# Performance work log

Hardware: AMD Instinct MI355X
Metric: run time of the kernel (lower is better)

Reference implementation:

```python
import jax, jax.numpy as jnp
import numpy as np

N, E, CIN, COUT = 50000, 800000, 61, 64
EPS = 1e-5


def batchnorm(h, g, b):
    # BatchNorm1d in training mode: batch stats (biased variance), affine
    m = jnp.mean(h, axis=0)
    v = jnp.var(h, axis=0)
    return g * (h - m) * jax.lax.rsqrt(v + EPS) + b


def setup_inputs() -> dict:
    key = jax.random.key(0)
    ks = jax.random.split(key, 7)
    x = jax.random.normal(ks[0], (N, CIN), jnp.float32)
    pos = jax.random.normal(ks[1], (N, 3), jnp.float32)
    edge_index = jax.random.randint(ks[2], (2, E), 0, N, dtype=jnp.int64)
    s1 = 1.0 / np.sqrt(CIN + 3)
    s2 = 1.0 / np.sqrt(COUT)
    ss = 1.0 / np.sqrt(CIN)
    W1 = jax.random.normal(ks[3], (CIN + 3, COUT), jnp.float32) * s1
    b1 = jnp.zeros((COUT,), jnp.float32)
    W2 = jax.random.normal(ks[4], (COUT, COUT), jnp.float32) * s2
    b2 = jnp.zeros((COUT,), jnp.float32)
    Ws = jax.random.normal(ks[5], (CIN, COUT), jnp.float32) * ss
    bs = jnp.zeros((COUT,), jnp.float32)
    ones = jnp.ones((COUT,), jnp.float32)
    zeros = jnp.zeros((COUT,), jnp.float32)
    return {
        "x": x, "pos": pos, "edge_index": edge_index,
        "W1": W1, "b1": b1, "g1": ones, "be1": zeros,
        "W2": W2, "b2": b2, "g2": ones, "be2": zeros,
        "Ws": Ws, "bs": bs, "gs": ones, "bes": zeros,
        "gf": ones, "bef": zeros,
    }


def reference(x, pos, edge_index, W1, b1, g1, be1, W2, b2, g2, be2,
              Ws, bs, gs, bes, gf, bef):
    src, dst = edge_index[0], edge_index[1]  # j -> i (source_to_target)
    # per-edge message: [x_j, pos_j - pos_i]  -> [E, CIN+3]
    msg = jnp.concatenate([x[src], pos[src] - pos[dst]], axis=-1)
    # local_nn = MLP([CIN+3, COUT, COUT]) with per-layer Lin -> ReLU -> BN
    h = batchnorm(jax.nn.relu(msg @ W1 + b1), g1, be1)
    h = batchnorm(jax.nn.relu(h @ W2 + b2), g2, be2)
    # scatter-max aggregation to destination nodes
    agg = jax.ops.segment_max(h, dst, num_segments=N)
    agg = jnp.where(jnp.isneginf(agg), 0.0, agg)  # nodes with no incoming edges
    # residual shortcut (Linear + BN since CIN != COUT)
    identity = batchnorm(x @ Ws + bs, gs, bes)
    return jax.nn.relu(batchnorm(agg, gf, bef) + identity)
```

## Files before the change

kernel.cpp:

```cpp
#include <hip/hip_runtime.h>

#define CIN 61
constexpr float EPS = 1e-5f;
constexpr double SCALE = 16777216.0;

using s16x8 = __attribute__((ext_vector_type(8))) short;
using fx4   = __attribute__((ext_vector_type(4))) float;

static __device__ __forceinline__ unsigned short f2bf(float f) {
  unsigned int u = __float_as_uint(f);
  u = (u + 0x7fffu + ((u >> 16) & 1u)) >> 16;
  return (unsigned short)u;
}
static __device__ __forceinline__ float bf2f(unsigned short h) {
  return __uint_as_float(((unsigned int)h) << 16);
}

__device__ __forceinline__ void stat_reduce(float val, float* red, long long* dst_ll) {
  int tid = threadIdx.x;
  red[tid] = val;
  __syncthreads();
  if (tid < 64) {
    float t = red[tid] + red[tid + 64] + red[tid + 128] + red[tid + 192];
    atomicAdd((unsigned long long*)&dst_ll[tid],
              (unsigned long long)(long long)((double)t * SCALE));
  }
  __syncthreads();
}

__global__ __launch_bounds__(256) void k_node(
    const float* __restrict__ x, const float* __restrict__ W1,
    const float* __restrict__ b1, const float* __restrict__ Ws,
    const float* __restrict__ bs, unsigned short* __restrict__ y,
    unsigned short* __restrict__ s_out, long long* __restrict__ stats, int N,
    const int* __restrict__ ei, unsigned int* __restrict__ hist,
    unsigned short* __restrict__ rank, int E) {
  const int tid = threadIdx.x, lane = tid & 63, wv = tid >> 6;
  float w1r[64], wsr[64];
#pragma unroll
  for (int k = 0; k < 64; ++k) {
    w1r[k] = (k < CIN) ? W1[k * 64 + lane] : 0.f;
    wsr[k] = (k < CIN) ? Ws[k * 64 + lane] : 0.f;
  }
  const float b1v = b1[lane], bsv = bs[lane];
  __shared__ float lrow[4][64];
  __shared__ float red[256];
  float ssum = 0.f, ssq = 0.f;
  const int nq = N >> 2;
  for (int q = blockIdx.x; q < nq; q += gridDim.x) {
    const int n = (q << 2) + wv;
    lrow[wv][lane] = (lane < CIN) ? x[(size_t)n * CIN + lane] : 0.f;
    __builtin_amdgcn_wave_barrier();
    float a0 = b1v, a1 = 0.f, a2 = 0.f, a3 = 0.f;
    float c0 = bsv, c1 = 0.f, c2 = 0.f, c3 = 0.f;
    const float4* rr = (const float4*)&lrow[wv][0];
#pragma unroll
    for (int k4 = 0; k4 < 16; ++k4) {
      float4 v = rr[k4];
      a0 = fmaf(v.x, w1r[4 * k4 + 0], a0);
      a1 = fmaf(v.y, w1r[4 * k4 + 1], a1);
      a2 = fmaf(v.z, w1r[4 * k4 + 2], a2);
      a3 = fmaf(v.w, w1r[4 * k4 + 3], a3);
      c0 = fmaf(v.x, wsr[4 * k4 + 0], c0);
      c1 = fmaf(v.y, wsr[4 * k4 + 1], c1);
      c2 = fmaf(v.z, wsr[4 * k4 + 2], c2);
      c3 = fmaf(v.w, wsr[4 * k4 + 3], c3);
    }
    y[(size_t)n * 64 + lane] = f2bf((a0 + a1) + (a2 + a3));
    const float sacc = (c0 + c1) + (c2 + c3);
    s_out[(size_t)n * 64 + lane] = f2bf(sacc);
    ssum += sacc;
    ssq = fmaf(sacc, sacc, ssq);
    __builtin_amdgcn_wave_barrier();
  }
  stat_reduce(ssum, red, stats + 256);
  stat_reduce(ssq, red, stats + 320);
  for (int i = blockIdx.x * 256 + tid; i < E; i += gridDim.x * 256) {
    const int dst = ei[E + i];
    rank[i] = (unsigned short)atomicAdd(&hist[dst], 1u);
  }
}

__global__ __launch_bounds__(256) void k_scan1(
    const unsigned int* __restrict__ hist, unsigned int* __restrict__ bsum) {
  const int tid = threadIdx.x, lane = tid & 63, wv = tid >> 6;
  const uint4 v = ((const uint4*)(hist + blockIdx.x * 1024))[tid];
  unsigned int s = v.x + v.y + v.z + v.w;
#pragma unroll
  for (int off = 1; off < 64; off <<= 1) s += __shfl_xor(s, off);
  __shared__ unsigned int wsum[4];
  if (lane == 0) wsum[wv] = s;
  __syncthreads();
  if (tid == 0) bsum[blockIdx.x] = wsum[0] + wsum[1] + wsum[2] + wsum[3];
}

__global__ void k_scan2(const unsigned int* __restrict__ bsum,
                        unsigned int* __restrict__ boff, int nb) {
  const int t = threadIdx.x;
  unsigned int v = (t < nb) ? bsum[t] : 0u;
  unsigned int incl = v;
#pragma unroll
  for (int off = 1; off < 64; off <<= 1) {
    unsigned int u = __shfl_up(incl, off);
    if (t >= off) incl += u;
  }
  if (t < nb) boff[t] = incl - v;
}

__global__ __launch_bounds__(256) void k_scan3(
    const unsigned int* __restrict__ hist, const unsigned int* __restrict__ boff,
    unsigned int* __restrict__ cursor0) {
  const int tid = threadIdx.x, lane = tid & 63, wv = tid >> 6;
  const uint4 v = ((const uint4*)(hist + blockIdx.x * 1024))[tid];
  const unsigned int s = v.x + v.y + v.z + v.w;
  unsigned int incl = s;
#pragma unroll
  for (int off = 1; off < 64; off <<= 1) {
    unsigned int u = __shfl_up(incl, off);
    if (lane >= off) incl += u;
  }
  __shared__ unsigned int wtot[4];
  if (lane == 63) wtot[wv] = incl;
  __syncthreads();
  unsigned int wb = boff[blockIdx.x];
#pragma unroll
  for (int k = 0; k < 4; ++k) wb += (k < wv) ? wtot[k] : 0u;
  const unsigned int ex = wb + incl - s;
  uint4 o;
  o.x = ex; o.y = ex + v.x; o.z = o.y + v.y; o.w = o.z + v.z;
  ((uint4*)(cursor0 + blockIdx.x * 1024))[tid] = o;
}

__global__ __launch_bounds__(256) void k_dstfill(
    const unsigned int* __restrict__ cursor0, unsigned short* __restrict__ dstS,
    int N) {
  const int d = blockIdx.x * 256 + threadIdx.x;
  if (d >= N) return;
  const unsigned int lo = cursor0[d];
  const unsigned int hi = cursor0[d + 1];
  for (unsigned int i = lo; i < hi; ++i) dstS[i] = (unsigned short)d;
}

__global__ __launch_bounds__(256) void k_edge1(
    const int* __restrict__ ei, const float* __restrict__ pos,
    const unsigned short* __restrict__ y, const float* __restrict__ W1,
    const unsigned int* __restrict__ cursor0, const unsigned short* __restrict__ rank,
    unsigned short* __restrict__ t1S, long long* __restrict__ stats, int E) {
  const int tid = threadIdx.x, lane = tid & 63, wv = tid >> 6;
  const int g8 = lane >> 3, c8 = lane & 7;
  float wp[3][8];
#pragma unroll
  for (int d = 0; d < 3; ++d)
#pragma unroll
    for (int i = 0; i < 8; ++i) wp[d][i] = W1[(61 + d) * 64 + 8 * c8 + i];
  float ssum[8] = {0.f, 0.f, 0.f, 0.f, 0.f, 0.f, 0.f, 0.f};
  float ssq[8]  = {0.f, 0.f, 0.f, 0.f, 0.f, 0.f, 0.f, 0.f};
  const int ngrp = E >> 3;
  const int nw = gridDim.x * 4;
  for (int q = blockIdx.x * 4 + wv; q < ngrp; q += 4 * nw) {
    const int qB = q + nw, qC = q + 2 * nw, qD = q + 3 * nw;
    const bool hB = qB < ngrp, hC = qC < ngrp, hD = qD < ngrp;
    const int eA = (q << 3) + g8;
    const int eB = hB ? (qB << 3) + g8 : eA;
    const int eC = hC ? (qC << 3) + g8 : eA;
    const int eD = hD ? (qD << 3) + g8 : eA;
    const int srcA = ei[eA], dstA = ei[E + eA];
    const int srcB = ei[eB], dstB = ei[E + eB];
    const int srcC = ei[eC], dstC = ei[E + eC];
    const int srcD = ei[eD], dstD = ei[E + eD];
    float pvA = 0.f, pvB = 0.f, pvC = 0.f, pvD = 0.f;
    if (c8 < 3) {
      pvA = pos[srcA * 3 + c8] - pos[dstA * 3 + c8];
      pvB = pos[srcB * 3 + c8] - pos[dstB * 3 + c8];
      pvC = pos[srcC * 3 + c8] - pos[dstC * 3 + c8];
      pvD = pos[srcD * 3 + c8] - pos[dstD * 3 + c8];
    }
    const s16x8 yA = *(const s16x8*)(y + (unsigned)srcA * 64u + 8u * (unsigned)c8);
    const s16x8 yB = *(const s16x8*)(y + (unsigned)srcB * 64u + 8u * (unsigned)c8);
    const s16x8 yC = *(const s16x8*)(y + (unsigned)srcC * 64u + 8u * (unsigned)c8);
    const s16x8 yD = *(const s16x8*)(y + (unsigned)srcD * 64u + 8u * (unsigned)c8);
    unsigned offA = 0, offB = 0, offC = 0, offD = 0;
    if (c8 == 0) {
      offA = cursor0[dstA] + rank[eA];
      offB = cursor0[dstB] + rank[eB];
      offC = cursor0[dstC] + rank[eC];
      offD = cursor0[dstD] + rank[eD];
    }
#define EDGE1_BODY(PV, YV, OFFV)                                                \
    {                                                                           \
      const float p0 = __shfl(PV, g8 * 8 + 0);                                  \
      const float p1 = __shfl(PV, g8 * 8 + 1);                                  \
      const float p2 = __shfl(PV, g8 * 8 + 2);                                  \
      const unsigned off = __shfl(OFFV, g8 * 8 + 0);                            \
      union { s16x8 v; unsigned short s[8]; } tb;                               \
      _Pragma("unroll")                                                         \
      for (int i = 0; i < 8; ++i) {                                             \
        float v = bf2f((unsigned short)YV[i]);                                  \
        v = fmaf(p0, wp[0][i], v);                                              \
        v = fmaf(p1, wp[1][i], v);                                              \
        v = fmaf(p2, wp[2][i], v);                                              \
        v = fmaxf(v, 0.f);                                                      \
        ssum[i] += v;                                                           \
        ssq[i] = fmaf(v, v, ssq[i]);                                            \
        tb.s[i] = f2bf(v);                                                      \
      }                                                                         \
      *(s16x8*)(t1S + (size_t)off * 64 + 8 * c8) = tb.v;                        \
    }
    EDGE1_BODY(pvA, yA, offA)
    if (hB) EDGE1_BODY(pvB, yB, offB)
    if (hC) EDGE1_BODY(pvC, yC, offC)
    if (hD) EDGE1_BODY(pvD, yD, offD)
#undef EDGE1_BODY
  }
#pragma unroll
  for (int i = 0; i < 8; ++i) {
    ssum[i] += __shfl_xor(ssum[i], 8);
    ssum[i] += __shfl_xor(ssum[i], 16);
    ssum[i] += __shfl_xor(ssum[i], 32);
    ssq[i] += __shfl_xor(ssq[i], 8);
    ssq[i] += __shfl_xor(ssq[i], 16);
    ssq[i] += __shfl_xor(ssq[i], 32);
  }
  __shared__ float sred[2][64];
  if (tid < 128) ((float*)sred)[tid] = 0.f;
  __syncthreads();
  if (g8 == 0) {
#pragma unroll
    for (int i = 0; i < 8; ++i) {
      atomicAdd(&sred[0][8 * c8 + i], ssum[i]);
      atomicAdd(&sred[1][8 * c8 + i], ssq[i]);
    }
  }
  __syncthreads();
  if (tid < 64) {
    atomicAdd((unsigned long long*)&stats[0 + tid],
              (unsigned long long)(long long)((double)sred[0][tid] * SCALE));
    atomicAdd((unsigned long long*)&stats[64 + tid],
              (unsigned long long)(long long)((double)sred[1][tid] * SCALE));
  }
}

__global__ void k_coefA(const long long* __restrict__ stats,
                        const float* __restrict__ g1, const float* __restrict__ be1,
                        const float* __restrict__ W2, const float* __restrict__ b2,
                        unsigned short* __restrict__ bFpack,
                        float* __restrict__ biasF, double invE) {
  const int c = threadIdx.x;
  __shared__ float a1s[64], c1s[64], b2sh[64];
  double m = (double)stats[c] * invE;
  double v = (double)stats[64 + c] * invE - m * m;
  float a = g1[c] * rsqrtf((float)v + EPS);
  a1s[c] = a;
  c1s[c] = fmaf(-(float)m, a, be1[c]);
  __syncthreads();
  float acc = b2[c];
  for (int k = 0; k < 64; ++k) acc = fmaf(c1s[k], W2[k * 64 + c], acc);
  b2sh[c] = acc;
  const int lg = c >> 4, l15 = c & 15;
#pragma unroll
  for (int t = 0; t < 4; ++t)
#pragma unroll
    for (int s = 0; s < 2; ++s)
#pragma unroll
      for (int i = 0; i < 8; ++i) {
        const int k = s * 32 + lg * 8 + i;
        bFpack[c * 64 + t * 16 + s * 8 + i] = f2bf(a1s[k] * W2[k * 64 + l15 + 16 * t]);
      }
  __syncthreads();
  float4 bf;
  bf.x = b2sh[l15]; bf.y = b2sh[l15 + 16]; bf.z = b2sh[l15 + 32]; bf.w = b2sh[l15 + 48];
  ((float4*)biasF)[c] = bf;
}

__global__ __launch_bounds__(256) void k_edge2(
    const unsigned short* __restrict__ t1S, const unsigned short* __restrict__ dstS,
    const unsigned short* __restrict__ bFpack, const float* __restrict__ biasF,
    long long* __restrict__ stats, unsigned int* __restrict__ agg, int E) {
  const int tid = threadIdx.x, lane = tid & 63, wv = tid >> 6;
  const int l15 = lane & 15, lg = lane >> 4;
  s16x8 bF[4][2];
  {
    const s16x8* bfp = (const s16x8*)(bFpack + (size_t)lane * 64);
#pragma unroll
    for (int t = 0; t < 4; ++t)
#pragma unroll
      for (int s = 0; s < 2; ++s) bF[t][s] = bfp[t * 2 + s];
  }
  float bias[4];
  {
    const float4 bv = ((const float4*)biasF)[lane];
    bias[0] = bv.x; bias[1] = bv.y; bias[2] = bv.z; bias[3] = bv.w;
  }
  __shared__ float ld2[4][16][68];
  float ssum[4] = {0.f, 0.f, 0.f, 0.f}, ssq[4] = {0.f, 0.f, 0.f, 0.f};
  const int nchunk = E >> 6;
  const int nw4 = gridDim.x * 4;
  for (int ch = blockIdx.x * 4 + wv; ch < nchunk; ch += nw4) {
    const int row0 = ch << 6;
    int cur = -1;
    float m = 0.f;
    bool inside = false;
#pragma unroll
    for (int t4 = 0; t4 < 4; ++t4) {
      const int rbase = row0 + (t4 << 4);
      const unsigned short* ar = t1S + (size_t)(rbase + l15) * 64 + (unsigned)(lg * 8);
      const s16x8 aF0 = *(const s16x8*)ar;
      const s16x8 aF1 = *(const s16x8*)(ar + 32);
      const int dstv = (int)dstS[rbase + l15];
      fx4 acc[4];
#pragma unroll
      for (int t = 0; t < 4; ++t) {
        acc[t][0] = bias[t]; acc[t][1] = bias[t];
        acc[t][2] = bias[t]; acc[t][3] = bias[t];
      }
#pragma unroll
      for (int t = 0; t < 4; ++t) {
        acc[t] = __builtin_amdgcn_mfma_f32_16x16x32_bf16(aF0, bF[t][0], acc[t], 0, 0, 0);
        acc[t] = __builtin_amdgcn_mfma_f32_16x16x32_bf16(aF1, bF[t][1], acc[t], 0, 0, 0);
      }
#pragma unroll
      for (int t = 0; t < 4; ++t) {
        const int col = l15 + 16 * t;
#pragma unroll
        for (int j = 0; j < 4; ++j) {
          const float v = fmaxf(acc[t][j], 0.f);
          ssum[t] += v;
          ssq[t] = fmaf(v, v, ssq[t]);
          ld2[wv][lg * 4 + j][col] = v;
        }
      }
      __builtin_amdgcn_wave_barrier();
      float v16[16];
#pragma unroll
      for (int r = 0; r < 16; ++r) v16[r] = ld2[wv][r][lane];
#pragma unroll
      for (int r = 0; r < 16; ++r) {
        const int d = __shfl(dstv, r);
        const float v = v16[r];
        if (d == cur) {
          m = fmaxf(m, v);
        } else {
          if (cur >= 0) {
            const unsigned int enc = __float_as_uint(m) | 0x80000000u;
            if (inside) agg[(unsigned)cur * 64u + lane] = enc;
            else atomicMax(&agg[(unsigned)cur * 64u + lane], enc);
          }
          cur = d;
          m = v;
          inside = (t4 > 0) || (r > 0);
        }
      }
      __builtin_amdgcn_wave_barrier();
    }
    if (cur >= 0)
      atomicMax(&agg[(unsigned)cur * 64u + lane], __float_as_uint(m) | 0x80000000u);
  }
#pragma unroll
  for (int t = 0; t < 4; ++t) {
    ssum[t] += __shfl_xor(ssum[t], 16); ssum[t] += __shfl_xor(ssum[t], 32);
    ssq[t]  += __shfl_xor(ssq[t], 16);  ssq[t]  += __shfl_xor(ssq[t], 32);
  }
  __shared__ float sred[2][64];
  if (tid < 128) ((float*)sred)[tid] = 0.f;
  __syncthreads();
  if (lg == 0) {
#pragma unroll
    for (int t = 0; t < 4; ++t) {
      atomicAdd(&sred[0][l15 + 16 * t], ssum[t]);
      atomicAdd(&sred[1][l15 + 16 * t], ssq[t]);
    }
  }
  __syncthreads();
  if (tid < 64) {
    atomicAdd((unsigned long long*)&stats[128 + tid],
              (unsigned long long)(long long)((double)sred[0][tid] * SCALE));
    atomicAdd((unsigned long long*)&stats[192 + tid],
              (unsigned long long)(long long)((double)sred[1][tid] * SCALE));
  }
}

__global__ __launch_bounds__(256) void k_aggfix(
    const unsigned int* __restrict__ agg, long long* __restrict__ stats, int total) {
  const int tid = threadIdx.x;
  __shared__ float red[256];
  float ssum = 0.f, ssq = 0.f, kcf = 0.f;
  const int step = gridDim.x * 256;
  for (int i = blockIdx.x * 256 + tid; i < total; i += step) {
    const unsigned int u = agg[i];
    if (u >> 31) {
      const float v = __uint_as_float(u & 0x7fffffffu);
      ssum += v;
      ssq = fmaf(v, v, ssq);
      if ((i & 63) == 0) kcf += 1.f;
    }
  }
  stat_reduce(ssum, red, stats + 384);
  stat_reduce(ssq, red, stats + 448);
  stat_reduce(kcf, red, stats + 512);
}

__global__ void k_coefB(const long long* __restrict__ stats,
                        const float* __restrict__ g2, const float* __restrict__ be2,
                        const float* __restrict__ gs, const float* __restrict__ bes,
                        const float* __restrict__ gf, const float* __restrict__ bef,
                        float* __restrict__ coef, double invE, double invN, int N) {
  const int c = threadIdx.x;
  double m2 = (double)stats[128 + c] * invE;
  double v2 = (double)stats[192 + c] * invE - m2 * m2;
  float a2 = g2[c] * rsqrtf((float)v2 + EPS);
  float c2 = fmaf(-(float)m2, a2, be2[c]);
  double mS = (double)stats[256 + c] * invN;
  double vS = (double)stats[320 + c] * invN - mS * mS;
  float aS = gs[c] * rsqrtf((float)vS + EPS);
  float cS = fmaf(-(float)mS, aS, bes[c]);
  double su = (double)stats[384 + c] / SCALE;
  double qu = (double)stats[448 + c] / SCALE;
  double K  = (double)stats[512] / SCALE;
  double sv = (double)a2 * su + (double)c2 * K;
  double qv = (double)a2 * a2 * qu + 2.0 * a2 * c2 * su + (double)c2 * c2 * K;
  double mv = sv / N;
  double vv = qv / N - mv * mv;
  float aF = gf[c] * rsqrtf((float)vv + EPS);
  float cF = fmaf(-(float)mv, aF, bef[c]);
  coef[c]       = aF * a2;
  coef[64 + c]  = fmaf(aF, c2, cF);
  coef[128 + c] = cF;
  coef[192 + c] = aS;
  coef[256 + c] = cS;
}

__global__ __launch_bounds__(256) void k_final(
    const unsigned int* __restrict__ agg, const unsigned short* __restrict__ sbuf,
    const float* __restrict__ coef, float* __restrict__ out, int total) {
  int i = blockIdx.x * 256 + threadIdx.x;
  if (i >= total) return;
  const int c = i & 63;
  const unsigned int u = agg[i];
  float base;
  if (u >> 31)
    base = fmaf(coef[c], __uint_as_float(u & 0x7fffffffu), coef[64 + c]);
  else
    base = coef[128 + c];
  const float sv = fmaf(coef[192 + c], bf2f(sbuf[i]), coef[256 + c]);
  out[i] = fmaxf(base + sv, 0.f);
}

extern "C" void kernel_launch(void* const* d_in, const int* in_sizes, int n_in,
                              void* d_out, int out_size, void* d_ws, size_t ws_size,
                              hipStream_t stream) {
  const float* x   = (const float*)d_in[0];
  const float* pos = (const float*)d_in[1];
  const int*   ei  = (const int*)d_in[2];
  const float* W1  = (const float*)d_in[3];
  const float* b1  = (const float*)d_in[4];
  const float* g1  = (const float*)d_in[5];
  const float* be1 = (const float*)d_in[6];
  const float* W2  = (const float*)d_in[7];
  const float* b2  = (const float*)d_in[8];
  const float* g2  = (const float*)d_in[9];
  const float* be2 = (const float*)d_in[10];
  const float* Ws  = (const float*)d_in[11];
  const float* bs  = (const float*)d_in[12];
  const float* gs  = (const float*)d_in[13];
  const float* bes = (const float*)d_in[14];
  const float* gf  = (const float*)d_in[15];
  const float* bef = (const float*)d_in[16];
  const int N = in_sizes[0] / CIN;
  const int E = in_sizes[2] / 2;

  char* ws = (char*)d_ws;
  const size_t o_stats = 0;
  const size_t o_bsum  = 4608;
  const size_t o_boff  = 5120;
  const size_t o_hist  = 8192;
  const size_t o_agg   = o_hist + 200704;
  const size_t zeroEnd = o_agg + (size_t)N * 256;
  const size_t o_curs0 = zeroEnd;
  const size_t o_coef  = o_curs0 + 200704;
  const size_t o_frag  = o_coef + 4096;
  const size_t o_rank  = o_frag + 12288;
  const size_t o_dstS  = o_rank + (size_t)E * 2;
  const size_t o_ybuf  = o_dstS + (size_t)E * 2;
  const size_t o_sbuf  = o_ybuf + (size_t)N * 128;
  const size_t o_t1S   = o_sbuf + (size_t)N * 128;

  long long* stats      = (long long*)(ws + o_stats);
  unsigned int* bsum    = (unsigned int*)(ws + o_bsum);
  unsigned int* boff    = (unsigned int*)(ws + o_boff);
  unsigned int* hist    = (unsigned int*)(ws + o_hist);
  unsigned int* agg     = (unsigned int*)(ws + o_agg);
  unsigned int* cursor0 = (unsigned int*)(ws + o_curs0);
  float* coef           = (float*)(ws + o_coef);
  unsigned short* bFpack= (unsigned short*)(ws + o_frag);
  float* biasF          = (float*)(ws + o_frag + 8192);
  unsigned short* rank  = (unsigned short*)(ws + o_rank);
  unsigned short* dstS  = (unsigned short*)(ws + o_dstS);
  unsigned short* ybuf  = (unsigned short*)(ws + o_ybuf);
  unsigned short* sbuf  = (unsigned short*)(ws + o_sbuf);
  unsigned short* t1S   = (unsigned short*)(ws + o_t1S);

  const double invE = 1.0 / (SCALE * (double)E);
  const double invN = 1.0 / (SCALE * (double)N);
  const int total = N * 64;
  const int nScanBlk = 49;

  hipMemsetAsync(d_ws, 0, zeroEnd, stream);

  hipLaunchKernelGGL(k_node, dim3(1024), dim3(256), 0, stream,
                     x, W1, b1, Ws, bs, ybuf, sbuf, stats, N, ei, hist, rank, E);
  hipLaunchKernelGGL(k_scan1, dim3(nScanBlk), dim3(256), 0, stream, hist, bsum);
  hipLaunchKernelGGL(k_scan2, dim3(1), dim3(64), 0, stream, bsum, boff, nScanBlk);
  hipLaunchKernelGGL(k_scan3, dim3(nScanBlk), dim3(256), 0, stream,
                     hist, boff, cursor0);
  hipLaunchKernelGGL(k_dstfill, dim3((N + 255) / 256), dim3(256), 0, stream,
                     cursor0, dstS, N);
  hipLaunchKernelGGL(k_edge1, dim3(2048), dim3(256), 0, stream,
                     ei, pos, ybuf, W1, cursor0, rank, t1S, stats, E);
  hipLaunchKernelGGL(k_coefA, dim3(1), dim3(64), 0, stream,
                     stats, g1, be1, W2, b2, bFpack, biasF, invE);
  hipLaunchKernelGGL(k_edge2, dim3(1563), dim3(256), 0, stream,
                     t1S, dstS, bFpack, biasF, stats, agg, E);
  hipLaunchKernelGGL(k_aggfix, dim3(1024), dim3(256), 0, stream, agg, stats, total);
  hipLaunchKernelGGL(k_coefB, dim3(1), dim3(64), 0, stream,
                     stats, g2, be2, gs, bes, gf, bef, coef, invE, invN, N);
  hipLaunchKernelGGL(k_final, dim3((total + 255) / 256), dim3(256), 0, stream,
                     agg, sbuf, coef, (float*)d_out, total);
}
```

Baseline: 277.6 us.

## Replace LDS-transposed serial segment scan with ballot-based in-register segment max

The edge2 kernel no longer stages each 16-row MFMA tile through shared memory and walks the rows one by one per lane. It finds segment boundaries with a ballot over the sorted destination ids. For each segment it reduces the max in registers using cross-lane shuffles, then issues one atomicMax per column. Work is now split into 16-edge tiles instead of 64-edge chunks, and the grid grows to 2048 blocks. The catch is that every segment, including ones fully inside a tile, now goes through an atomic, and the per-segment loop costs extra shuffles.

Result: faster. 262.9 us (-5.3%).

```diff
diff --git a/kernel.cpp b/kernel.cpp
--- a/kernel.cpp
+++ b/kernel.cpp
@@ -291,69 +291,61 @@
     const float4 bv = ((const float4*)biasF)[lane];
     bias[0] = bv.x; bias[1] = bv.y; bias[2] = bv.z; bias[3] = bv.w;
   }
-  __shared__ float ld2[4][16][68];
   float ssum[4] = {0.f, 0.f, 0.f, 0.f}, ssq[4] = {0.f, 0.f, 0.f, 0.f};
-  const int nchunk = E >> 6;
-  const int nw4 = gridDim.x * 4;
-  for (int ch = blockIdx.x * 4 + wv; ch < nchunk; ch += nw4) {
-    const int row0 = ch << 6;
-    int cur = -1;
-    float m = 0.f;
-    bool inside = false;
-#pragma unroll
-    for (int t4 = 0; t4 < 4; ++t4) {
-      const int rbase = row0 + (t4 << 4);
-      const unsigned short* ar = t1S + (size_t)(rbase + l15) * 64 + (unsigned)(lg * 8);
-      const s16x8 aF0 = *(const s16x8*)ar;
-      const s16x8 aF1 = *(const s16x8*)(ar + 32);
-      const int dstv = (int)dstS[rbase + l15];
-      fx4 acc[4];
+  const int ntile = E >> 4;
+  const int nw = gridDim.x * 4;
+  for (int tile = blockIdx.x * 4 + wv; tile < ntile; tile += nw) {
+    const int rbase = tile << 4;
+    const unsigned short* ar = t1S + (size_t)(rbase + l15) * 64 + (unsigned)(lg * 8);
+    const s16x8 aF0 = *(const s16x8*)ar;
+    const s16x8 aF1 = *(const s16x8*)(ar + 32);
+    const int dstv = (int)dstS[rbase + l15];
+    fx4 acc[4];
+#pragma unroll
+    for (int t = 0; t < 4; ++t) {
+      acc[t][0] = bias[t]; acc[t][1] = bias[t];
+      acc[t][2] = bias[t]; acc[t][3] = bias[t];
+    }
+#pragma unroll
+    for (int t = 0; t < 4; ++t) {
+      acc[t] = __builtin_amdgcn_mfma_f32_16x16x32_bf16(aF0, bF[t][0], acc[t], 0, 0, 0);
+      acc[t] = __builtin_amdgcn_mfma_f32_16x16x32_bf16(aF1, bF[t][1], acc[t], 0, 0, 0);
+    }
+    float tv[4][4];
+#pragma unroll
+    for (int t = 0; t < 4; ++t)
+#pragma unroll
+      for (int j = 0; j < 4; ++j) {
+        const float v = fmaxf(acc[t][j], 0.f);
+        tv[t][j] = v;
+        ssum[t] += v;
+        ssq[t] = fmaf(v, v, ssq[t]);
+      }
+    const int prev = __shfl(dstv, (l15 + 15) & 15);
+    const bool isb = (l15 == 0) || (dstv != prev);
+    unsigned long long bm = __ballot(isb) & 0xFFFFull;
+    while (bm) {
+      const int r0 = __ffsll((long long)bm) - 1;
+      bm &= bm - 1;
+      const int r1 = bm ? (__ffsll((long long)bm) - 1) : 16;
+      const int d = __shfl(dstv, r0);
+      float lm[4];
 #pragma unroll
       for (int t = 0; t < 4; ++t) {
-        acc[t][0] = bias[t]; acc[t][1] = bias[t];
-        acc[t][2] = bias[t]; acc[t][3] = bias[t];
+        float m0 = 0.f;
+#pragma unroll
+        for (int j = 0; j < 4; ++j) {
+          const int row = lg * 4 + j;
+          m0 = fmaxf(m0, (row >= r0 && row < r1) ? tv[t][j] : 0.f);
+        }
+        m0 = fmaxf(m0, __shfl_xor(m0, 16));
+        m0 = fmaxf(m0, __shfl_xor(m0, 32));
+        lm[t] = m0;
       }
-#pragma unroll
-      for (int t = 0; t < 4; ++t) {
-        acc[t] = __builtin_amdgcn_mfma_f32_16x16x32_bf16(aF0, bF[t][0], acc[t], 0, 0, 0);
-        acc[t] = __builtin_amdgcn_mfma_f32_16x16x32_bf16(aF1, bF[t][1], acc[t], 0, 0, 0);
-      }
-#pragma unroll
-      for (int t = 0; t < 4; ++t) {
-        const int col = l15 + 16 * t;
-#pragma unroll
-        for (int j = 0; j < 4; ++j) {
-          const float v = fmaxf(acc[t][j], 0.f);
-          ssum[t] += v;
-          ssq[t] = fmaf(v, v, ssq[t]);
-          ld2[wv][lg * 4 + j][col] = v;
-        }
-      }
-      __builtin_amdgcn_wave_barrier();
-      float v16[16];
-#pragma unroll
-      for (int r = 0; r < 16; ++r) v16[r] = ld2[wv][r][lane];
-#pragma unroll
-      for (int r = 0; r < 16; ++r) {
-        const int d = __shfl(dstv, r);
-        const float v = v16[r];
-        if (d == cur) {
-          m = fmaxf(m, v);
-        } else {
-          if (cur >= 0) {
-            const unsigned int enc = __float_as_uint(m) | 0x80000000u;
-            if (inside) agg[(unsigned)cur * 64u + lane] = enc;
-            else atomicMax(&agg[(unsigned)cur * 64u + lane], enc);
-          }
-          cur = d;
-          m = v;
-          inside = (t4 > 0) || (r > 0);
-        }
-      }
-      __builtin_amdgcn_wave_barrier();
-    }
-    if (cur >= 0)
-      atomicMax(&agg[(unsigned)cur * 64u + lane], __float_as_uint(m) | 0x80000000u);
+      const float val = (lg == 0) ? lm[0] : (lg == 1) ? lm[1] : (lg == 2) ? lm[2] : lm[3];
+      atomicMax(&agg[(unsigned)d * 64u + (unsigned)(l15 + 16 * lg)],
+                __float_as_uint(val) | 0x80000000u);
+    }
   }
 #pragma unroll
   for (int t = 0; t < 4; ++t) {
@@ -518,7 +510,7 @@
                      ei, pos, ybuf, W1, cursor0, rank, t1S, stats, E);
   hipLaunchKernelGGL(k_coefA, dim3(1), dim3(64), 0, stream,
                      stats, g1, be1, W2, b2, bFpack, biasF, invE);
-  hipLaunchKernelGGL(k_edge2, dim3(1563), dim3(256), 0, stream,
+  hipLaunchKernelGGL(k_edge2, dim3(2048), dim3(256), 0, stream,
                      t1S, dstS, bFpack, biasF, stats, agg, E);
   hipLaunchKernelGGL(k_aggfix, dim3(1024), dim3(256), 0, stream, agg, stats, total);
   hipLaunchKernelGGL(k_coefB, dim3(1), dim3(64), 0, stream,
```
